# Kernel optimization log

Hardware: AMD Instinct MI355X
Metric: run time of the kernel (lower is better)

The kernel has to match this reference:

```python
import jax, jax.numpy as jnp
import numpy as np

EMBED_DIM = 1024
NUM_HEADS = 16
HEAD_DIM = EMBED_DIM // NUM_HEADS
MAX_DIST = 128
NUM_BUCKETS = 2 * MAX_DIST + 1  # 257: fixes off-by-one in original Embedding sizing


def setup_inputs() -> dict:
    key = jax.random.key(0)
    ks = jax.random.split(key, 10)
    B, S, D = 2, 2048, EMBED_DIM
    s = 1.0 / np.sqrt(D)
    return {
        "x": jax.random.normal(ks[0], (B, S, D), dtype=jnp.float32),
        "Wq": jax.random.normal(ks[1], (D, D), dtype=jnp.float32) * s,
        "bq": jnp.zeros((D,), dtype=jnp.float32),
        "Wk": jax.random.normal(ks[2], (D, D), dtype=jnp.float32) * s,
        "bk": jnp.zeros((D,), dtype=jnp.float32),
        "Wv": jax.random.normal(ks[3], (D, D), dtype=jnp.float32) * s,
        "bv": jnp.zeros((D,), dtype=jnp.float32),
        "Wo": jax.random.normal(ks[4], (D, D), dtype=jnp.float32) * s,
        "bo": jnp.zeros((D,), dtype=jnp.float32),
        "rel_emb": jax.random.normal(ks[5], (NUM_BUCKETS, NUM_HEADS), dtype=jnp.float32) * 0.02,
    }


def _rel_bias(rel_emb, seq_len):
    # relative position clamped to [-MAX_DIST, MAX_DIST], shifted to [0, 2*MAX_DIST]
    pos = jnp.arange(seq_len)
    rel = jnp.clip(pos[:, None] - pos[None, :], -MAX_DIST, MAX_DIST) + MAX_DIST
    bias = rel_emb[rel]                    # [S, S, H]
    return jnp.transpose(bias, (2, 0, 1))  # [H, S, S]


def reference(x, Wq, bq, Wk, bk, Wv, bv, Wo, bo, rel_emb):
    B, S, D = x.shape
    H, Hd = NUM_HEADS, HEAD_DIM
    # torch Linear: y = x @ W.T + b
    q = (x @ Wq.T + bq).reshape(B, S, H, Hd).transpose(0, 2, 1, 3)  # [B,H,S,Hd]
    k = (x @ Wk.T + bk).reshape(B, S, H, Hd).transpose(0, 2, 1, 3)
    v = (x @ Wv.T + bv).reshape(B, S, H, Hd).transpose(0, 2, 1, 3)
    scores = jnp.einsum("bhqd,bhkd->bhqk", q, k) / jnp.sqrt(jnp.float32(Hd))
    scores = scores + _rel_bias(rel_emb, S)[None]  # add [H,S,S] bias
    probs = jax.nn.softmax(scores, axis=-1)
    out = jnp.einsum("bhqk,bhkd->bhqd", probs, v)
    out = out.transpose(0, 2, 1, 3).reshape(B, S, D)
    return out @ Wo.T + bo
```

## Files before the change

### kernel.cpp

```cpp
#include <hip/hip_runtime.h>
#include <hip/hip_bf16.h>
#include <cstdint>
#include <cstddef>

#define DEVI __device__ __forceinline__

static constexpr int SEQ = 2048;
static constexpr int DM  = 1024;
static constexpr int NH  = 16;
static constexpr int HD  = 64;
static constexpr int NTOK = 2 * SEQ;
static constexpr int NBUCKET = 257;
static constexpr float LOG2E = 1.44269504088896f;

typedef __attribute__((ext_vector_type(8))) short bf16x8;
typedef __attribute__((ext_vector_type(4))) float f32x4;
#define MFMA16(a, b, c) __builtin_amdgcn_mfma_f32_16x16x32_bf16((a), (b), (c), 0, 0, 0)

DEVI float bf1(uint16_t u)  { return __uint_as_float(((uint32_t)u) << 16); }
DEVI uint16_t f2bf(float f) {
    uint32_t x = __float_as_uint(f);
    x += 0x7fffu + ((x >> 16) & 1u);
    return (uint16_t)(x >> 16);
}
DEVI bf16x8 ld_frag(const uint16_t* p) {
    union { uint4 u; bf16x8 f; } c;
    c.u = *(const uint4*)p;
    return c.f;
}
DEVI void gld16(const uint16_t* g, uint16_t* l) {
    __builtin_amdgcn_global_load_lds(
        (const __attribute__((address_space(1))) uint32_t*)g,
        (__attribute__((address_space(3))) uint32_t*)l, 16, 0, 0);
}

__global__ void sniff_kernel(const uint16_t* __restrict__ x, int* __restrict__ flag)
{
    int bad = 0;
    for (int i = threadIdx.x; i < 512; i += 64) {
        const float v = bf1(x[i]);
        if (!(fabsf(v) < 64.0f)) bad = 1;
    }
    const unsigned long long m = __ballot(bad);
    if (threadIdx.x == 0) *flag = (m != 0ull) ? 1 : 0;
}

__global__ __launch_bounds__(256)
void convert_kernel(const void* __restrict__ x, const void* __restrict__ Wq,
                    const void* __restrict__ Wk, const void* __restrict__ Wv,
                    const void* __restrict__ Wo, const void* __restrict__ bq,
                    const void* __restrict__ bk, const void* __restrict__ bv,
                    const void* __restrict__ bo, uint16_t* __restrict__ dst,
                    const int* __restrict__ flagp)
{
    const bool f32in = (*flagp != 0);
    const size_t M4 = 4194304, M1 = 1048576;
    const size_t e = ((size_t)blockIdx.x * 256 + threadIdx.x) * 8;
    const void* src; size_t off;
    if      (e < M4)                 { src = x;  off = e; }
    else if (e < M4 + M1)            { src = Wq; off = e - M4; }
    else if (e < M4 + 2*M1)          { src = Wk; off = e - M4 - M1; }
    else if (e < M4 + 3*M1)          { src = Wv; off = e - M4 - 2*M1; }
    else if (e < M4 + 4*M1)          { src = Wo; off = e - M4 - 3*M1; }
    else if (e < M4 + 4*M1 + 1024)   { src = bq; off = e - M4 - 4*M1; }
    else if (e < M4 + 4*M1 + 2048)   { src = bk; off = e - M4 - 4*M1 - 1024; }
    else if (e < M4 + 4*M1 + 3072)   { src = bv; off = e - M4 - 4*M1 - 2048; }
    else                             { src = bo; off = e - M4 - 4*M1 - 3072; }
    if (f32in) {
        const float4 a = *(const float4*)((const float*)src + off);
        const float4 b = *(const float4*)((const float*)src + off + 4);
        uint4 o;
        o.x = (uint32_t)f2bf(a.x) | ((uint32_t)f2bf(a.y) << 16);
        o.y = (uint32_t)f2bf(a.z) | ((uint32_t)f2bf(a.w) << 16);
        o.z = (uint32_t)f2bf(b.x) | ((uint32_t)f2bf(b.y) << 16);
        o.w = (uint32_t)f2bf(b.z) | ((uint32_t)f2bf(b.w) << 16);
        *(uint4*)(dst + e) = o;
    } else {
        *(uint4*)(dst + e) = *(const uint4*)((const uint16_t*)src + off);
    }
}

__global__ __launch_bounds__(256)
void gemm_qkv(const uint16_t* __restrict__ xc, const uint16_t* __restrict__ Wqkv,
              const uint16_t* __restrict__ bqkv,
              uint16_t* __restrict__ Qw, uint16_t* __restrict__ Kw,
              uint16_t* __restrict__ Vt)
{
    __shared__ uint16_t As[128 * 32];
    __shared__ uint16_t Bs[128 * 32];
    const int tid = threadIdx.x, bx = blockIdx.x;
    const int lane = tid & 63, wave = tid >> 6;
    const int ln = lane & 15, quad = lane >> 4;
    const int wm = (wave & 1) * 64, wn = (wave >> 1) * 64;

    const uint16_t *Ab, *Bb;
    int bm, bn, vor;
    if (bx < 512) {
        vor = 0; bm = (bx >> 4) * 128; bn = (bx & 15) * 128;
        Ab = xc + (size_t)bm * DM;  Bb = Wqkv + (size_t)bn * DM;
    } else {
        vor = 1; const int b2 = bx - 512; bm = (b2 >> 5) * 128; bn = (b2 & 31) * 128;
        Ab = Wqkv + (size_t)(2048 + bm) * DM;  Bb = xc + (size_t)bn * DM;
    }

    f32x4 acc[4][4];
    #pragma unroll
    for (int i = 0; i < 4; ++i)
        #pragma unroll
        for (int j = 0; j < 4; ++j) acc[i][j] = (f32x4){0.f, 0.f, 0.f, 0.f};

    const int s0 = tid, s1 = 256 + tid;
    const uint16_t* ga0 = Ab + (size_t)(s0 >> 2) * DM + (s0 & 3) * 8;
    const uint16_t* ga1 = Ab + (size_t)(s1 >> 2) * DM + (s1 & 3) * 8;
    const uint16_t* gb0 = Bb + (size_t)(s0 >> 2) * DM + (s0 & 3) * 8;
    const uint16_t* gb1 = Bb + (size_t)(s1 >> 2) * DM + (s1 & 3) * 8;

    for (int k0 = 0; k0 < DM; k0 += 32) {
        __syncthreads();
        gld16(ga0 + k0, &As[s0 * 8]);
        gld16(ga1 + k0, &As[s1 * 8]);
        gld16(gb0 + k0, &Bs[s0 * 8]);
        gld16(gb1 + k0, &Bs[s1 * 8]);
        __syncthreads();

        bf16x8 af[4], bfr[4];
        #pragma unroll
        for (int t = 0; t < 4; ++t) {
            af[t]  = ld_frag(&As[(wm + t * 16 + ln) * 32 + quad * 8]);
            bfr[t] = ld_frag(&Bs[(wn + t * 16 + ln) * 32 + quad * 8]);
        }
        #pragma unroll
        for (int ti = 0; ti < 4; ++ti)
            #pragma unroll
            for (int tj = 0; tj < 4; ++tj)
                acc[ti][tj] = MFMA16(af[ti], bfr[tj], acc[ti][tj]);
    }

    if (!vor) {
        #pragma unroll
        for (int tj = 0; tj < 4; ++tj) {
            const int c = bn + wn + tj * 16 + ln;
            const int mat = c >> 10, h = (c >> 6) & 15, hd = c & 63;
            uint16_t* dstp = mat ? Kw : Qw;
            const float scale = mat ? 1.0f : (0.125f * LOG2E);
            const float bb = bf1(bqkv[c]);
            #pragma unroll
            for (int ti = 0; ti < 4; ++ti)
                #pragma unroll
                for (int r = 0; r < 4; ++r) {
                    const int row = bm + wm + ti * 16 + quad * 4 + r;
                    const int b = row >> 11, s = row & 2047;
                    dstp[(((size_t)b * NH + h) * SEQ + s) * HD + hd] =
                        f2bf((acc[ti][tj][r] + bb) * scale);
                }
        }
    } else {
        #pragma unroll
        for (int ti = 0; ti < 4; ++ti)
            #pragma unroll
            for (int r = 0; r < 4; ++r) {
                const int f = bm + wm + ti * 16 + quad * 4 + r;
                const int h = f >> 6, hd = f & 63;
                const float bb = bf1(bqkv[2048 + f]);
                #pragma unroll
                for (int tj = 0; tj < 4; ++tj) {
                    const int t = bn + wn + tj * 16 + ln;
                    const int b = t >> 11, s = t & 2047;
                    Vt[(((size_t)b * NH + h) * HD + hd) * SEQ + s] = f2bf(acc[ti][tj][r] + bb);
                }
            }
    }
}

__global__ __launch_bounds__(256)
void gemm_out(const uint16_t* __restrict__ Cw, const uint16_t* __restrict__ Woc,
              const uint16_t* __restrict__ boc, void* __restrict__ out,
              const int* __restrict__ flagp)
{
    __shared__ uint16_t As[128 * 32];
    __shared__ uint16_t Bs[64 * 32];
    const int tid = threadIdx.x, bx = blockIdx.x;
    const int lane = tid & 63, wave = tid >> 6;
    const int ln = lane & 15, quad = lane >> 4;
    const int wm = (wave & 1) * 64, wn = (wave >> 1) * 32;
    const int bm = (bx >> 4) * 128, bn = (bx & 15) * 64;
    const uint16_t* Ab = Cw + (size_t)bm * DM;
    const uint16_t* Bb = Woc + (size_t)bn * DM;

    f32x4 acc[4][2];
    #pragma unroll
    for (int i = 0; i < 4; ++i)
        #pragma unroll
        for (int j = 0; j < 2; ++j) acc[i][j] = (f32x4){0.f, 0.f, 0.f, 0.f};

    const int s0 = tid, s1 = 256 + tid;
    const uint16_t* ga0 = Ab + (size_t)(s0 >> 2) * DM + (s0 & 3) * 8;
    const uint16_t* ga1 = Ab + (size_t)(s1 >> 2) * DM + (s1 & 3) * 8;
    const uint16_t* gb0 = Bb + (size_t)(s0 >> 2) * DM + (s0 & 3) * 8;

    for (int k0 = 0; k0 < DM; k0 += 32) {
        __syncthreads();
        gld16(ga0 + k0, &As[s0 * 8]);
        gld16(ga1 + k0, &As[s1 * 8]);
        gld16(gb0 + k0, &Bs[s0 * 8]);
        __syncthreads();

        bf16x8 af[4], bfr[2];
        #pragma unroll
        for (int t = 0; t < 4; ++t)
            af[t] = ld_frag(&As[(wm + t * 16 + ln) * 32 + quad * 8]);
        #pragma unroll
        for (int t = 0; t < 2; ++t)
            bfr[t] = ld_frag(&Bs[(wn + t * 16 + ln) * 32 + quad * 8]);
        #pragma unroll
        for (int ti = 0; ti < 4; ++ti)
            #pragma unroll
            for (int tj = 0; tj < 2; ++tj)
                acc[ti][tj] = MFMA16(af[ti], bfr[tj], acc[ti][tj]);
    }

    const bool f32o = (*flagp != 0);
    #pragma unroll
    for (int tj = 0; tj < 2; ++tj) {
        const int c = bn + wn + tj * 16 + ln;
        const float bb = bf1(boc[c]);
        #pragma unroll
        for (int ti = 0; ti < 4; ++ti)
            #pragma unroll
            for (int r = 0; r < 4; ++r) {
                const int row = bm + wm + ti * 16 + quad * 4 + r;
                const float v = acc[ti][tj][r] + bb;
                if (f32o) ((float*)out)[(size_t)row * DM + c] = v;
                else      ((uint16_t*)out)[(size_t)row * DM + c] = f2bf(v);
            }
    }
}

__global__ __launch_bounds__(256, 4)
void attn_mfma(const uint16_t* __restrict__ Q, const uint16_t* __restrict__ K,
               const uint16_t* __restrict__ Vt, const void* __restrict__ rel,
               uint16_t* __restrict__ ctx, const int* __restrict__ flagp)
{
    __shared__ alignas(16) uint16_t Ks[64 * 64];
    __shared__ alignas(16) uint16_t Vls[64 * 64];
    __shared__ alignas(16) uint16_t Pl[4][16 * 64];
    __shared__ float bias_s[NBUCKET];

    const bool f32in = (*flagp != 0);
    const int tid = threadIdx.x, wave = tid >> 6, lane = tid & 63;
    const int ln = lane & 15, quad = lane >> 4;

    const int blk = blockIdx.x;
    const int bh = (blk & 7) * 4 + ((blk >> 3) & 3);
    const int qt = blk >> 5;
    const int b = bh >> 4, h = bh & 15;
    const int q0 = qt * 64;

    const float C8 = 8.0f * LOG2E;
    for (int i = tid; i < NBUCKET; i += 256) {
        const float bv = f32in ? ((const float*)rel)[i * NH + h]
                               : bf1(((const uint16_t*)rel)[i * NH + h]);
        bias_s[i] = bv * LOG2E - C8;
    }
    __syncthreads();
    const float bneg = bias_s[0], bpos = bias_s[256];

    const uint16_t* qp = Q + ((size_t)bh * SEQ + q0 + wave * 16 + ln) * HD;
    const bf16x8 qf0 = ld_frag(qp + quad * 8);
    const bf16x8 qf1 = ld_frag(qp + 32 + quad * 8);

    union { uint4 u; bf16x8 f; } onec;
    onec.u = (uint4){0x3F803F80u, 0x3F803F80u, 0x3F803F80u, 0x3F803F80u};
    const bf16x8 onef = onec.f;

    f32x4 o[4];
    f32x4 lf = (f32x4){0.f, 0.f, 0.f, 0.f};
    #pragma unroll
    for (int dt = 0; dt < 4; ++dt) o[dt] = (f32x4){0.f, 0.f, 0.f, 0.f};

    const uint16_t* Kb  = K  + (size_t)bh * SEQ * HD;
    const uint16_t* Vtb = Vt + (size_t)bh * HD * SEQ;
    const int swz = ln & 7;
    uint16_t* myP = Pl[wave];

    const int s_0 = tid, s_1 = 256 + tid;
    const int r_0 = s_0 >> 3, c_0 = (s_0 & 7) ^ (r_0 & 7);
    const int r_1 = s_1 >> 3, c_1 = (s_1 & 7) ^ (r_1 & 7);
    const int koff0 = r_0 * HD + c_0 * 8,  koff1 = r_1 * HD + c_1 * 8;
    const int voff0 = r_0 * SEQ + c_0 * 8, voff1 = r_1 * SEQ + c_1 * 8;
    uint16_t* const kl0 = &Ks[s_0 * 8];
    uint16_t* const kl1 = &Ks[s_1 * 8];
    uint16_t* const vl0 = &Vls[s_0 * 8];
    uint16_t* const vl1 = &Vls[s_1 * 8];

    const uint16_t* kfp[4][2];
    const uint16_t* vfp[4][2];
    #pragma unroll
    for (int t = 0; t < 4; ++t) {
        const int row = (t * 16 + ln) * 64;
        kfp[t][0] = &Ks[row + ((0 + quad) ^ swz) * 8];
        kfp[t][1] = &Ks[row + ((4 + quad) ^ swz) * 8];
        vfp[t][0] = &Vls[row + ((0 + quad) ^ swz) * 8];
        vfp[t][1] = &Vls[row + ((4 + quad) ^ swz) * 8];
    }
    uint16_t* Pw[4];
    #pragma unroll
    for (int nt = 0; nt < 4; ++nt) {
        const int cb = (2 * nt + (quad >> 1)) ^ swz;
        Pw[nt] = &myP[ln * 64 + cb * 8 + (quad & 1) * 4];
    }
    const uint16_t* const pfp0 = &myP[ln * 64 + ((0 + quad) ^ swz) * 8];
    const uint16_t* const pfp1 = &myP[ln * 64 + ((4 + quad) ^ swz) * 8];

    const uint16_t* kgb = Kb;
    const uint16_t* vgb = Vtb;

    for (int k0 = 0; k0 < SEQ; k0 += 64) {
        __syncthreads();
        gld16(kgb + koff0, kl0);
        gld16(kgb + koff1, kl1);
        gld16(vgb + voff0, vl0);
        gld16(vgb + voff1, vl1);
        kgb += 64 * HD; vgb += 64;
        __syncthreads();

        const int mode = (k0 >= q0 + 192) ? 0 : ((k0 + 192 <= q0) ? 2 : 1);

        if (mode != 1) {
            const float binit = (mode == 0) ? bneg : bpos;
            #pragma unroll
            for (int nt = 0; nt < 4; ++nt) {
                const bf16x8 kf0 = ld_frag(kfp[nt][0]);
                const bf16x8 kf1 = ld_frag(kfp[nt][1]);
                f32x4 s4 = (f32x4){binit, binit, binit, binit};
                s4 = MFMA16(kf0, qf0, s4);
                s4 = MFMA16(kf1, qf1, s4);
                uint32_t pb[4];
                #pragma unroll
                for (int r = 0; r < 4; ++r)
                    pb[r] = __float_as_uint(exp2f(s4[r]));
                const uint2 dw = {__builtin_amdgcn_perm(pb[1], pb[0], 0x07060302u),
                                  __builtin_amdgcn_perm(pb[3], pb[2], 0x07060302u)};
                *(uint2*)Pw[nt] = dw;
            }
        } else {
            const int iq = q0 + wave * 16 + ln + 128 - k0 - quad * 4;
            #pragma unroll
            for (int nt = 0; nt < 4; ++nt) {
                const bf16x8 kf0 = ld_frag(kfp[nt][0]);
                const bf16x8 kf1 = ld_frag(kfp[nt][1]);
                f32x4 s4 = (f32x4){0.f, 0.f, 0.f, 0.f};
                s4 = MFMA16(kf0, qf0, s4);
                s4 = MFMA16(kf1, qf1, s4);
                uint32_t pb[4];
                #pragma unroll
                for (int r = 0; r < 4; ++r) {
                    int x = iq - (nt * 16 + r);
                    x = max(0, min(256, x));
                    pb[r] = __float_as_uint(exp2f(s4[r] + bias_s[x]));
                }
                const uint2 dw = {__builtin_amdgcn_perm(pb[1], pb[0], 0x07060302u),
                                  __builtin_amdgcn_perm(pb[3], pb[2], 0x07060302u)};
                *(uint2*)Pw[nt] = dw;
            }
        }

        const bf16x8 pf0 = ld_frag(pfp0);
        const bf16x8 pf1 = ld_frag(pfp1);
        lf = MFMA16(pf0, onef, lf);
        lf = MFMA16(pf1, onef, lf);
        #pragma unroll
        for (int dt = 0; dt < 4; ++dt) {
            o[dt] = MFMA16(pf0, ld_frag(vfp[dt][0]), o[dt]);
            o[dt] = MFMA16(pf1, ld_frag(vfp[dt][1]), o[dt]);
        }
    }

    #pragma unroll
    for (int r = 0; r < 4; ++r) {
        const float inv = 1.0f / lf[r];
        const int qq = q0 + wave * 16 + quad * 4 + r;
        #pragma unroll
        for (int dt = 0; dt < 4; ++dt)
            ctx[(((size_t)b * SEQ + qq) * NH + h) * HD + dt * 16 + ln] =
                f2bf(o[dt][r] * inv);
    }
}

extern "C" void kernel_launch(void* const* d_in, const int* in_sizes, int n_in,
                              void* d_out, int out_size, void* d_ws, size_t ws_size,
                              hipStream_t stream)
{
    const void* x   = d_in[0];
    const void* Wq  = d_in[1];
    const void* bq  = d_in[2];
    const void* Wk  = d_in[3];
    const void* bk  = d_in[4];
    const void* Wv  = d_in[5];
    const void* bv  = d_in[6];
    const void* Wo  = d_in[7];
    const void* bo  = d_in[8];
    const void* rel = d_in[9];

    const size_t M4 = 4194304, M1 = 1048576;
    uint16_t* ws16 = (uint16_t*)d_ws;
    uint16_t* xc   = ws16;
    uint16_t* Wqkv = ws16 + M4;
    uint16_t* Woc  = ws16 + M4 + 3 * M1;
    uint16_t* bqkv = ws16 + M4 + 4 * M1;
    uint16_t* boc  = bqkv + 3072;
    uint16_t* Qw   = ws16 + M4 + 4 * M1 + 8192;
    uint16_t* Kw   = Qw + M4;
    uint16_t* Vt   = Kw + M4;
    int* flag = (int*)(Vt + M4);
    uint16_t* Cw = xc;

    sniff_kernel<<<1, 64, 0, stream>>>((const uint16_t*)x, flag);
    convert_kernel<<<4098, 256, 0, stream>>>(x, Wq, Wk, Wv, Wo, bq, bk, bv, bo,
                                             ws16, flag);
    gemm_qkv<<<768, 256, 0, stream>>>(xc, Wqkv, bqkv, Qw, Kw, Vt);
    attn_mfma<<<1024, 256, 0, stream>>>(Qw, Kw, Vt, rel, Cw, flag);
    gemm_out<<<512, 256, 0, stream>>>(Cw, Woc, boc, d_out, flag);
}
```

Baseline: 229.3 us.

## Double-buffer K/V tiles and process 128 queries per attention block

The attention kernel now uses 512-thread blocks covering 128 query rows, so each K/V tile loaded into shared memory is reused by twice as many waves. K/V shared buffers are doubled: the next tile's load is issued before the current tile's compute, which removes one of the two barriers per tile. Bias-mode thresholds are adjusted for the taller query tile, and exp2f is swapped for the hardware exp2 builtin. The main risk is register pressure, since launch bounds of 512 threads with 4 blocks per CU may force spills. Fewer blocks may also lower occupancy.

```diff
diff --git a/kernel.cpp b/kernel.cpp
--- a/kernel.cpp
+++ b/kernel.cpp
@@ -236,14 +236,66 @@
     }
 }
 
-__global__ __launch_bounds__(256, 4)
+#define ATTN_COMPUTE(K0, KSB, VSB)                                             \
+  do {                                                                         \
+    const int mode_ = ((K0) >= q0 + 256) ? 0 : (((K0) + 192 <= q0) ? 2 : 1);   \
+    if (mode_ != 1) {                                                          \
+      const float binit_ = (mode_ == 0) ? bneg : bpos;                         \
+      _Pragma("unroll")                                                        \
+      for (int nt = 0; nt < 4; ++nt) {                                         \
+        const bf16x8 kf0 = ld_frag((KSB) + kvo[nt][0]);                        \
+        const bf16x8 kf1 = ld_frag((KSB) + kvo[nt][1]);                        \
+        f32x4 s4 = (f32x4){binit_, binit_, binit_, binit_};                    \
+        s4 = MFMA16(kf0, qf0, s4);                                             \
+        s4 = MFMA16(kf1, qf1, s4);                                             \
+        uint32_t pb[4];                                                        \
+        _Pragma("unroll")                                                      \
+        for (int r = 0; r < 4; ++r)                                            \
+          pb[r] = __float_as_uint(__builtin_amdgcn_exp2f(s4[r]));              \
+        const uint2 dw = {__builtin_amdgcn_perm(pb[1], pb[0], 0x07060302u),    \
+                          __builtin_amdgcn_perm(pb[3], pb[2], 0x07060302u)};   \
+        *(uint2*)Pw[nt] = dw;                                                  \
+      }                                                                        \
+    } else {                                                                   \
+      const int iq_ = q0 + wave * 16 + ln + 128 - (K0) - quad * 4;             \
+      _Pragma("unroll")                                                        \
+      for (int nt = 0; nt < 4; ++nt) {                                         \
+        const bf16x8 kf0 = ld_frag((KSB) + kvo[nt][0]);                        \
+        const bf16x8 kf1 = ld_frag((KSB) + kvo[nt][1]);                        \
+        f32x4 s4 = (f32x4){0.f, 0.f, 0.f, 0.f};                                \
+        s4 = MFMA16(kf0, qf0, s4);                                             \
+        s4 = MFMA16(kf1, qf1, s4);                                             \
+        uint32_t pb[4];                                                        \
+        _Pragma("unroll")                                                      \
+        for (int r = 0; r < 4; ++r) {                                          \
+          int x_ = iq_ - (nt * 16 + r);                                        \
+          x_ = max(0, min(256, x_));                                           \
+          pb[r] = __float_as_uint(__builtin_amdgcn_exp2f(s4[r] + bias_s[x_])); \
+        }                                                                      \
+        const uint2 dw = {__builtin_amdgcn_perm(pb[1], pb[0], 0x07060302u),    \
+                          __builtin_amdgcn_perm(pb[3], pb[2], 0x07060302u)};   \
+        *(uint2*)Pw[nt] = dw;                                                  \
+      }                                                                        \
+    }                                                                          \
+    const bf16x8 pf0 = ld_frag(pfp0);                                          \
+    const bf16x8 pf1 = ld_frag(pfp1);                                          \
+    lf = MFMA16(pf0, onef, lf);                                                \
+    lf = MFMA16(pf1, onef, lf);                                                \
+    _Pragma("unroll")                                                          \
+    for (int dt = 0; dt < 4; ++dt) {                                           \
+      o[dt] = MFMA16(pf0, ld_frag((VSB) + kvo[dt][0]), o[dt]);                 \
+      o[dt] = MFMA16(pf1, ld_frag((VSB) + kvo[dt][1]), o[dt]);                 \
+    }                                                                          \
+  } while (0)
+
+__global__ __launch_bounds__(512, 4)
 void attn_mfma(const uint16_t* __restrict__ Q, const uint16_t* __restrict__ K,
                const uint16_t* __restrict__ Vt, const void* __restrict__ rel,
                uint16_t* __restrict__ ctx, const int* __restrict__ flagp)
 {
-    __shared__ alignas(16) uint16_t Ks[64 * 64];
-    __shared__ alignas(16) uint16_t Vls[64 * 64];
-    __shared__ alignas(16) uint16_t Pl[4][16 * 64];
+    __shared__ alignas(16) uint16_t Ks[2][64 * 64];
+    __shared__ alignas(16) uint16_t Vls[2][64 * 64];
+    __shared__ alignas(16) uint16_t Pl[8][16 * 64];
     __shared__ float bias_s[NBUCKET];
 
     const bool f32in = (*flagp != 0);
@@ -254,16 +306,14 @@
     const int bh = (blk & 7) * 4 + ((blk >> 3) & 3);
     const int qt = blk >> 5;
     const int b = bh >> 4, h = bh & 15;
-    const int q0 = qt * 64;
+    const int q0 = qt * 128;
 
     const float C8 = 8.0f * LOG2E;
-    for (int i = tid; i < NBUCKET; i += 256) {
+    for (int i = tid; i < NBUCKET; i += 512) {
         const float bv = f32in ? ((const float*)rel)[i * NH + h]
                                : bf1(((const uint16_t*)rel)[i * NH + h]);
         bias_s[i] = bv * LOG2E - C8;
     }
-    __syncthreads();
-    const float bneg = bias_s[0], bpos = bias_s[256];
 
     const uint16_t* qp = Q + ((size_t)bh * SEQ + q0 + wave * 16 + ln) * HD;
     const bf16x8 qf0 = ld_frag(qp + quad * 8);
@@ -278,30 +328,26 @@
     #pragma unroll
     for (int dt = 0; dt < 4; ++dt) o[dt] = (f32x4){0.f, 0.f, 0.f, 0.f};
 
-    const uint16_t* Kb  = K  + (size_t)bh * SEQ * HD;
-    const uint16_t* Vtb = Vt + (size_t)bh * HD * SEQ;
     const int swz = ln & 7;
     uint16_t* myP = Pl[wave];
 
-    const int s_0 = tid, s_1 = 256 + tid;
-    const int r_0 = s_0 >> 3, c_0 = (s_0 & 7) ^ (r_0 & 7);
-    const int r_1 = s_1 >> 3, c_1 = (s_1 & 7) ^ (r_1 & 7);
-    const int koff0 = r_0 * HD + c_0 * 8,  koff1 = r_1 * HD + c_1 * 8;
-    const int voff0 = r_0 * SEQ + c_0 * 8, voff1 = r_1 * SEQ + c_1 * 8;
-    uint16_t* const kl0 = &Ks[s_0 * 8];
-    uint16_t* const kl1 = &Ks[s_1 * 8];
-    uint16_t* const vl0 = &Vls[s_0 * 8];
-    uint16_t* const vl1 = &Vls[s_1 * 8];
-
-    const uint16_t* kfp[4][2];
-    const uint16_t* vfp[4][2];
+    const int r_ = tid >> 3, c_ = (tid & 7) ^ (r_ & 7);
+    const int koff = r_ * HD + c_ * 8;
+    const int voff = r_ * SEQ + c_ * 8;
+    uint16_t* const kd0 = &Ks[0][tid * 8];
+    uint16_t* const kd1 = &Ks[1][tid * 8];
+    uint16_t* const vd0 = &Vls[0][tid * 8];
+    uint16_t* const vd1 = &Vls[1][tid * 8];
+
+    const uint16_t* kg = K  + (size_t)bh * SEQ * HD + koff;
+    const uint16_t* vg = Vt + (size_t)bh * HD * SEQ + voff;
+
+    int kvo[4][2];
     #pragma unroll
     for (int t = 0; t < 4; ++t) {
         const int row = (t * 16 + ln) * 64;
-        kfp[t][0] = &Ks[row + ((0 + quad) ^ swz) * 8];
-        kfp[t][1] = &Ks[row + ((4 + quad) ^ swz) * 8];
-        vfp[t][0] = &Vls[row + ((0 + quad) ^ swz) * 8];
-        vfp[t][1] = &Vls[row + ((4 + quad) ^ swz) * 8];
+        kvo[t][0] = row + ((0 + quad) ^ swz) * 8;
+        kvo[t][1] = row + ((4 + quad) ^ swz) * 8;
     }
     uint16_t* Pw[4];
     #pragma unroll
@@ -312,68 +358,23 @@
     const uint16_t* const pfp0 = &myP[ln * 64 + ((0 + quad) ^ swz) * 8];
     const uint16_t* const pfp1 = &myP[ln * 64 + ((4 + quad) ^ swz) * 8];
 
-    const uint16_t* kgb = Kb;
-    const uint16_t* vgb = Vtb;
-
-    for (int k0 = 0; k0 < SEQ; k0 += 64) {
-        __syncthreads();
-        gld16(kgb + koff0, kl0);
-        gld16(kgb + koff1, kl1);
-        gld16(vgb + voff0, vl0);
-        gld16(vgb + voff1, vl1);
-        kgb += 64 * HD; vgb += 64;
-        __syncthreads();
-
-        const int mode = (k0 >= q0 + 192) ? 0 : ((k0 + 192 <= q0) ? 2 : 1);
-
-        if (mode != 1) {
-            const float binit = (mode == 0) ? bneg : bpos;
-            #pragma unroll
-            for (int nt = 0; nt < 4; ++nt) {
-                const bf16x8 kf0 = ld_frag(kfp[nt][0]);
-                const bf16x8 kf1 = ld_frag(kfp[nt][1]);
-                f32x4 s4 = (f32x4){binit, binit, binit, binit};
-                s4 = MFMA16(kf0, qf0, s4);
-                s4 = MFMA16(kf1, qf1, s4);
-                uint32_t pb[4];
-                #pragma unroll
-                for (int r = 0; r < 4; ++r)
-                    pb[r] = __float_as_uint(exp2f(s4[r]));
-                const uint2 dw = {__builtin_amdgcn_perm(pb[1], pb[0], 0x07060302u),
-                                  __builtin_amdgcn_perm(pb[3], pb[2], 0x07060302u)};
-                *(uint2*)Pw[nt] = dw;
-            }
-        } else {
-            const int iq = q0 + wave * 16 + ln + 128 - k0 - quad * 4;
-            #pragma unroll
-            for (int nt = 0; nt < 4; ++nt) {
-                const bf16x8 kf0 = ld_frag(kfp[nt][0]);
-                const bf16x8 kf1 = ld_frag(kfp[nt][1]);
-                f32x4 s4 = (f32x4){0.f, 0.f, 0.f, 0.f};
-                s4 = MFMA16(kf0, qf0, s4);
-                s4 = MFMA16(kf1, qf1, s4);
-                uint32_t pb[4];
-                #pragma unroll
-                for (int r = 0; r < 4; ++r) {
-                    int x = iq - (nt * 16 + r);
-                    x = max(0, min(256, x));
-                    pb[r] = __float_as_uint(exp2f(s4[r] + bias_s[x]));
-                }
-                const uint2 dw = {__builtin_amdgcn_perm(pb[1], pb[0], 0x07060302u),
-                                  __builtin_amdgcn_perm(pb[3], pb[2], 0x07060302u)};
-                *(uint2*)Pw[nt] = dw;
-            }
+    gld16(kg, kd0); gld16(vg, vd0);
+    kg += 64 * HD; vg += 64;
+    __syncthreads();
+    const float bneg = bias_s[0], bpos = bias_s[256];
+
+    for (int t = 0; t < 16; ++t) {
+        gld16(kg, kd1); gld16(vg, vd1);
+        kg += 64 * HD; vg += 64;
+        ATTN_COMPUTE(t * 128, &Ks[0][0], &Vls[0][0]);
+        __syncthreads();
+
+        if (t < 15) {
+            gld16(kg, kd0); gld16(vg, vd0);
+            kg += 64 * HD; vg += 64;
         }
-
-        const bf16x8 pf0 = ld_frag(pfp0);
-        const bf16x8 pf1 = ld_frag(pfp1);
-        lf = MFMA16(pf0, onef, lf);
-        lf = MFMA16(pf1, onef, lf);
-        #pragma unroll
-        for (int dt = 0; dt < 4; ++dt) {
-            o[dt] = MFMA16(pf0, ld_frag(vfp[dt][0]), o[dt]);
-            o[dt] = MFMA16(pf1, ld_frag(vfp[dt][1]), o[dt]);
-        }
+        ATTN_COMPUTE(t * 128 + 64, &Ks[1][0], &Vls[1][0]);
+        __syncthreads();
     }
 
     #pragma unroll
@@ -419,6 +420,6 @@
     convert_kernel<<<4098, 256, 0, stream>>>(x, Wq, Wk, Wv, Wo, bq, bk, bv, bo,
                                              ws16, flag);
     gemm_qkv<<<768, 256, 0, stream>>>(xc, Wqkv, bqkv, Qw, Kw, Vt);
-    attn_mfma<<<1024, 256, 0, stream>>>(Qw, Kw, Vt, rel, Cw, flag);
+    attn_mfma<<<512, 512, 0, stream>>>(Qw, Kw, Vt, rel, Cw, flag);
     gemm_out<<<512, 256, 0, stream>>>(Cw, Woc, boc, d_out, flag);
 }
```

Result: faster. 207.4 us (-9.6%).
